# Kernel optimization log

Hardware: AMD Instinct MI355X
Metric: run time of the kernel (lower is better)

Reference implementation:

```python
import jax, jax.numpy as jnp
import numpy as np

N, NB, NP, T = 1024, 16, 256, 80
EPS_LEN = 1e-9   # seg_len clamp_min in original
EPS_DD = 1e-12   # dot(d,d) clamp_min in original


def setup_inputs() -> dict:
    key = jax.random.key(0)
    k1, k2, k3, k4 = jax.random.split(key, 4)
    # smooth-ish random trajectory (cumsum of steps)
    selected_traj = jnp.cumsum(jax.random.normal(k1, (N, T, 3), jnp.float32) * 0.5, axis=1)
    # random polylines per (sample, boundary)
    road_points = jnp.cumsum(jax.random.normal(k2, (N, NB, NP, 3), jnp.float32) * 0.5, axis=2) \
                  + jax.random.normal(k3, (N, NB, 1, 3), jnp.float32) * 2.0
    # ragged valid-prefix masks, length in [2, NP]
    lengths = jax.random.randint(k4, (N, NB), 2, NP + 1)
    road_mask = jnp.arange(NP)[None, None, :] < lengths[:, :, None]
    return {"selected_traj": selected_traj, "road_points": road_points, "road_mask": road_mask}


def _arc_project(pos, rp, rm):
    # pos: [N,T,3]; rp: [N,NB,NP,3]; rm: [N,NB,NP] bool
    n, t = pos.shape[0], pos.shape[1]
    nb, npts = rp.shape[1], rp.shape[2]
    inf = jnp.asarray(jnp.inf, pos.dtype)
    ar = jnp.arange(npts)
    n_valid = rm.sum(-1)                                    # [N,NB]

    # pack valid points to the front, preserving order (== boolean-mask gather in torch)
    order = jnp.argsort(jnp.logical_not(rm), axis=-1, stable=True)
    pts_f = jnp.take_along_axis(rp, order[..., None], axis=2)      # [N,NB,NP,3]
    pack_mask = ar[None, None, :] < n_valid[:, :, None]
    pts_f = jnp.where(pack_mask[..., None], pts_f, 0.0)
    # flipped direction: reverse the valid prefix
    flip_idx = jnp.clip(n_valid[:, :, None] - 1 - ar[None, None, :], 0, npts - 1)
    pts_b = jnp.take_along_axis(pts_f, flip_idx[..., None], axis=2)
    pts_b = jnp.where(pack_mask[..., None], pts_b, 0.0)
    pts = jnp.stack([pts_f, pts_b], axis=2)                 # [N,NB,2,NP,3]

    # segment i is real iff i < n_valid-1
    seg_mask = ar[: npts - 1][None, None, None, :] < (n_valid - 1)[:, :, None, None]  # [N,NB,1,NP-1]
    seg_vec = pts[..., 1:, :] - pts[..., :-1, :]            # [N,NB,2,NP-1,3]
    seg_norm = jnp.sqrt((seg_vec ** 2).sum(-1))
    seg_len = jnp.where(seg_mask, jnp.maximum(seg_norm, EPS_LEN), 0.0)
    cum_s = jnp.concatenate([jnp.zeros_like(seg_len[..., :1]), jnp.cumsum(seg_len, -1)], -1)  # [N,NB,2,NP]
    last_idx = jnp.clip(n_valid - 1, 0, npts - 1)[:, :, None, None]
    total_s = jnp.take_along_axis(cum_s, jnp.broadcast_to(last_idx, (n, nb, 2, 1)), -1)  # [N,NB,2,1]

    # entry: project first trajectory point onto nearest valid segment
    p0 = pos[:, 0][:, None, None, None, :]                  # [N,1,1,1,3]
    a0 = pts[..., :-1, :]
    dd0 = jnp.maximum((seg_vec ** 2).sum(-1), EPS_DD)
    t0 = jnp.clip(((p0 - a0) * seg_vec).sum(-1) / dd0, 0.0, 1.0)
    q0 = a0 + t0[..., None] * seg_vec
    d2 = jnp.where(seg_mask, ((p0 - q0) ** 2).sum(-1), inf)
    seg0 = jnp.argmin(d2, -1)[..., None]                    # [N,NB,2,1]
    entry_s = jnp.take_along_axis(cum_s, seg0, -1) + jnp.take_along_axis(t0 * seg_len, seg0, -1)

    # trajectory arc-length, resample polyline at entry_s + traj arc length
    traj_seg = jnp.sqrt(((pos[:, 1:] - pos[:, :-1]) ** 2).sum(-1))
    traj_cs = jnp.concatenate([jnp.zeros_like(traj_seg[:, :1]), jnp.cumsum(traj_seg, -1)], -1)  # [N,T]
    target_s = jnp.clip(entry_s + traj_cs[:, None, None, :], 0.0, total_s)  # [N,NB,2,T]

    j = jax.vmap(lambda c, tg: jnp.searchsorted(c, tg, side='right'))(
        cum_s.reshape(-1, npts), target_s.reshape(-1, t)) - 1
    j = jnp.clip(j.reshape(n, nb, 2, t), 0, jnp.maximum(n_valid[:, :, None, None] - 2, 0))

    seg_l = jnp.take_along_axis(seg_len, j, -1)
    cs_j = jnp.take_along_axis(cum_s, j, -1)
    t_loc = jnp.clip((target_s - cs_j) / jnp.maximum(seg_l, EPS_LEN), 0.0, 1.0)
    pa = jnp.take_along_axis(pts, j[..., None], axis=3)
    pb = jnp.take_along_axis(pts, (j + 1)[..., None], axis=3)
    proj = pa + t_loc[..., None] * (pb - pa)                # [N,NB,2,T,3]

    # pick (boundary, direction) candidate with min total L2 cost
    cost = jnp.sqrt(((pos[:, None, None] - proj) ** 2).sum(-1)).sum(-1)  # [N,NB,2]
    cand_ok = (n_valid >= 2)[:, :, None]
    cost = jnp.where(cand_ok, cost, inf)
    best = jnp.argmin(cost.reshape(n, -1), -1)
    best_proj = jnp.take_along_axis(proj.reshape(n, -1, t, 3), best[:, None, None, None], axis=1)[:, 0]
    has = cand_ok.any((1, 2))
    return jnp.where(has[:, None, None], best_proj, pos)


def reference(selected_traj, road_points, road_mask):
    pos = selected_traj[..., 0:3]
    out_pos = _arc_project(pos, road_points, road_mask)
    return jnp.concatenate([out_pos, selected_traj[..., 3:]], axis=-1)
```

## Files before the change

kernel.cpp:

```cpp
#include <hip/hip_runtime.h>
#include <math.h>

#define NN 1024
#define NBB 16
#define NP 256
#define TT 80
#define EPS_LEN 1e-9f
#define EPS_DD 1e-12f

__device__ __forceinline__ float frcp(float x){ return __builtin_amdgcn_rcpf(x); }
__device__ __forceinline__ float fsq(float x){ return __builtin_amdgcn_sqrtf(x); }
__device__ __forceinline__ float rlane_f(float x, int l){
  return __builtin_bit_cast(float, __builtin_amdgcn_readlane(__builtin_bit_cast(int, x), l));
}

template<int CTRL,int RM>
__device__ __forceinline__ float dpp_add(float v){
  int t = __builtin_amdgcn_update_dpp(0, __builtin_bit_cast(int, v), CTRL, RM, 0xf, true);
  return v + __builtin_bit_cast(float, t);
}
__device__ __forceinline__ float wave_incl_scan(float v){
  v = dpp_add<0x111,0xf>(v);
  v = dpp_add<0x112,0xf>(v);
  v = dpp_add<0x114,0xf>(v);
  v = dpp_add<0x118,0xf>(v);
  v = dpp_add<0x142,0xa>(v);
  v = dpp_add<0x143,0xc>(v);
  return v;
}
__device__ __forceinline__ float wave_sum(float v){ return rlane_f(wave_incl_scan(v), 63); }
template<int CTRL,int RM>
__device__ __forceinline__ float dpp_min(float v){
  int t = __builtin_amdgcn_update_dpp(0x7f800000, __builtin_bit_cast(int,v), CTRL, RM, 0xf, false);
  return fminf(v, __builtin_bit_cast(float,t));
}
__device__ __forceinline__ float wave_min_all(float v){
  v=dpp_min<0x111,0xf>(v); v=dpp_min<0x112,0xf>(v);
  v=dpp_min<0x114,0xf>(v); v=dpp_min<0x118,0xf>(v);
  v=dpp_min<0x142,0xa>(v); v=dpp_min<0x143,0xc>(v);
  return rlane_f(v, 63);
}

__device__ __forceinline__ void lds_fence() {
  __builtin_amdgcn_wave_barrier();
  asm volatile("s_waitcnt lgkmcnt(0)" ::: "memory");
  __builtin_amdgcn_wave_barrier();
}

__device__ __forceinline__ int wave_nv(const void* mask, size_t base, int lane) {
  bool as_byte = ((const unsigned char*)mask)[1] != 0;
  int nv = 0;
  if (as_byte) {
    uchar4 v = ((const uchar4*)((const unsigned char*)mask + base))[lane];
    nv += __popcll(__ballot(v.x != 0));
    nv += __popcll(__ballot(v.y != 0));
    nv += __popcll(__ballot(v.z != 0));
    nv += __popcll(__ballot(v.w != 0));
  } else {
    int4 v = ((const int4*)((const int*)mask + base))[lane];
    nv += __popcll(__ballot(v.x != 0));
    nv += __popcll(__ballot(v.y != 0));
    nv += __popcll(__ballot(v.z != 0));
    nv += __popcll(__ballot(v.w != 0));
  }
  return nv;
}

template<bool STRICT>
__device__ __forceinline__ int count256(const float* __restrict__ cs,
                                        const float* co, float v){
  int K = 0;
  #pragma unroll
  for (int k=0;k<16;k++) K += STRICT ? (co[k] < v) : (co[k] <= v);
  int base = (K < 16 ? K : 15) * 16;
  const float4* f4 = (const float4*)(cs + base);
  float4 c0=f4[0], c1=f4[1], c2=f4[2], c3=f4[3];
  int r;
  if (STRICT)
    r = (c0.x<v)+(c0.y<v)+(c0.z<v)+(c0.w<v)+(c1.x<v)+(c1.y<v)+(c1.z<v)+(c1.w<v)
      + (c2.x<v)+(c2.y<v)+(c2.z<v)+(c2.w<v)+(c3.x<v)+(c3.y<v)+(c3.z<v)+(c3.w<v);
  else
    r = (c0.x<=v)+(c0.y<=v)+(c0.z<=v)+(c0.w<=v)+(c1.x<=v)+(c1.y<=v)+(c1.z<=v)+(c1.w<=v)
      + (c2.x<=v)+(c2.y<=v)+(c2.z<=v)+(c2.w<=v)+(c3.x<=v)+(c3.y<=v)+(c3.z<=v)+(c3.w<=v);
  return (K >= 16) ? 256 : (base + r);
}

struct SegOut {
  float cpre[4];
  float run;
  float bdf, btf; int bjf;
  float bdl, btl; int bjl;
};

template<bool NEEDMIN>
__device__ __forceinline__ void seg_pass(const float4* __restrict__ p4, int lane, int nv,
                                         float p0x, float p0y, float p0z,
                                         float* __restrict__ pts, SegOut& R) {
  const int j0 = lane * 4;
  float4 A = make_float4(0.f,0.f,0.f,0.f), B = A, C = A;
  if (j0 < nv) { A = p4[lane*3+0]; B = p4[lane*3+1]; C = p4[lane*3+2]; }
  float x[5], y[5], z[5];
  x[0]=A.x; y[0]=A.y; z[0]=A.z;
  x[1]=A.w; y[1]=B.x; z[1]=B.y;
  x[2]=B.z; y[2]=B.w; z[2]=C.x;
  x[3]=C.y; y[3]=C.z; z[3]=C.w;
  x[4]=__shfl_down(x[0],1,64); y[4]=__shfl_down(y[0],1,64); z[4]=__shfl_down(z[0],1,64);
  ((float4*)pts)[lane*3+0] = make_float4(x[0],y[0],z[0],x[1]);
  ((float4*)pts)[lane*3+1] = make_float4(y[1],z[1],x[2],y[2]);
  ((float4*)pts)[lane*3+2] = make_float4(z[2],x[3],y[3],z[3]);
  float run = 0.f;
  R.bdf=INFINITY; R.btf=0.f; R.bjf=j0;
  R.bdl=INFINITY; R.btl=0.f; R.bjl=j0;
  #pragma unroll
  for (int k=0;k<4;k++){
    bool valid = (j0+k) < nv-1;
    float vx=x[k+1]-x[k], vy=y[k+1]-y[k], vz=z[k+1]-z[k];
    float n2 = vx*vx+vy*vy+vz*vz;
    float sl = valid ? fmaxf(fsq(n2), EPS_LEN) : 0.f;
    if (NEEDMIN){
      float t = ((p0x-x[k])*vx+(p0y-y[k])*vy+(p0z-z[k])*vz) * frcp(fmaxf(n2,EPS_DD));
      t = fminf(fmaxf(t,0.f),1.f);
      float qx=x[k]+t*vx, qy=y[k]+t*vy, qz=z[k]+t*vz;
      float dx=p0x-qx, dy=p0y-qy, dz=p0z-qz;
      float d2 = valid ? (dx*dx+dy*dy+dz*dz) : INFINITY;
      if (d2 <  R.bdf){R.bdf=d2; R.bjf=j0+k; R.btf=t;}
      if (d2 <= R.bdl){R.bdl=d2; R.bjl=j0+k; R.btl=t;}
    }
    run += sl; R.cpre[k]=run;
  }
  R.run = run;
}

__device__ __forceinline__ void cs_pair_from_regs(int idx, float ex, const SegOut& R,
                                                  float& c0, float& c1){
  int o = idx >> 2, r = idx & 3;
  float a0 = (r==0)?0.f : (r==1)?R.cpre[0] : (r==2)?R.cpre[1] : R.cpre[2];
  float a1 = (r==0)?R.cpre[0] : (r==1)?R.cpre[1] : (r==2)?R.cpre[2] : R.run;
  c0 = rlane_f(ex + a0, o);
  c1 = rlane_f(ex + a1, o);
}

__device__ __forceinline__ void interp_at(const float* __restrict__ pts,
                                          const float* __restrict__ cs,
                                          const float* co, float Tot, int nv, int jmaxv,
                                          int dir, float ts,
                                          float& prx, float& pry, float& prz){
  int ia, ib; float tl;
  if (dir){
    float v = Tot - ts;
    int lb = count256<true>(cs, co, v);
    int j = nv-1-lb; j = j<0?0:(j>jmaxv?jmaxv:j);
    int l2 = nv-1-j;
    float base = Tot - cs[l2];
    tl = (ts-base)*frcp(fmaxf(cs[l2]-cs[l2-1], EPS_LEN));
    ia=l2; ib=l2-1;
  } else {
    int ub = count256<false>(cs, co, ts);
    int j = ub-1; j = j<0?0:(j>jmaxv?jmaxv:j);
    tl = (ts - cs[j])*frcp(fmaxf(cs[j+1]-cs[j], EPS_LEN));
    ia=j; ib=j+1;
  }
  tl = fminf(fmaxf(tl,0.f),1.f);
  float3 PA = *(const float3*)(pts + ia*3);
  float3 PB = *(const float3*)(pts + ib*3);
  prx = PA.x + tl*(PB.x-PA.x);
  pry = PA.y + tl*(PB.y-PA.y);
  prz = PA.z + tl*(PB.z-PA.z);
}

__device__ void eval_cost_wave(float* __restrict__ pts, float* __restrict__ cs,
                               const float* __restrict__ pos, const float* __restrict__ tc,
                               const float4* __restrict__ p4, int nv,
                               float* __restrict__ cost2, float2* __restrict__ ent2){
  const int lane = threadIdx.x & 63;
  float l_tc[3];
  #pragma unroll
  for (int p=0;p<3;p++){
    int task = p*64 + lane;
    int r = task>=TT ? task-TT : task;
    int t = (r<TT) ? r : 0;
    l_tc[p] = tc[t];
  }
  SegOut R;
  seg_pass<true>(p4, lane, nv, pos[0], pos[1], pos[2], pts, R);

  float inc = wave_incl_scan(R.run);
  float ex = inc - R.run;
  ((float4*)cs)[lane] = make_float4(ex, ex+R.cpre[0], ex+R.cpre[1], ex+R.cpre[2]);
  const float Tot = rlane_f(inc, 63);

  float cval = ex + R.cpre[2];
  float co[16];
  #pragma unroll
  for (int k=0;k<16;k++) co[k] = rlane_f(cval, 4*k+3);

  float minv = wave_min_all(R.bdf);
  unsigned long long mf = __ballot(R.bdf == minv);
  unsigned long long ml = __ballot(R.bdl == minv);
  int lf = __builtin_ctzll(mf);
  int ll = 63 - __builtin_clzll(ml);
  int   jf = __builtin_amdgcn_readlane(R.bjf, lf);
  float tf = rlane_f(R.btf, lf);
  int   jl = __builtin_amdgcn_readlane(R.bjl, ll);
  float tl0 = rlane_f(R.btl, ll);

  float cjf, cjf1, cjl, cjl1;
  cs_pair_from_regs(jf, ex, R, cjf, cjf1);
  cs_pair_from_regs(jl, ex, R, cjl, cjl1);
  float e0 = cjf + tf*(cjf1-cjf);
  float e1 = (Tot - cjl1) + (1.f-tl0)*(cjl1-cjl);

  lds_fence();

  const int jmaxv = nv-2;
  float accf=0.f, accr=0.f;
  #pragma unroll
  for (int p=0;p<3;p++){
    int task = p*64 + lane;
    bool act = task < 2*TT;
    int dir = task>=TT ? 1 : 0;
    int t = dir ? task-TT : task;
    float ts = (dir ? e1 : e0) + l_tc[p];
    ts = fminf(fmaxf(ts,0.f),Tot);
    float prx,pry,prz;
    interp_at(pts, cs, co, Tot, nv, jmaxv, dir, ts, prx,pry,prz);
    if (act){
      float dx=pos[t*3+0]-prx, dy=pos[t*3+1]-pry, dz=pos[t*3+2]-prz;
      float dd=fsq(dx*dx+dy*dy+dz*dz);
      if (dir) accr+=dd; else accf+=dd;
    }
  }
  float cf = wave_sum(accf), cr = wave_sum(accr);
  if (lane==0){
    cost2[0]=cf; cost2[1]=cr;
    *ent2 = make_float2(e0, e1);
  }
}

__device__ void eval_proj_wave(float* __restrict__ pts, float* __restrict__ cs,
                               const float* __restrict__ tc,
                               const float4* __restrict__ p4, int nv,
                               int wdir, float entry, float* __restrict__ out){
  const int lane = threadIdx.x & 63;
  float l_tc[2];
  #pragma unroll
  for (int p=0;p<2;p++){
    int t = p*64 + lane;
    l_tc[p] = tc[(t<TT)?t:0];
  }
  SegOut R;
  seg_pass<false>(p4, lane, nv, 0.f,0.f,0.f, pts, R);
  float inc = wave_incl_scan(R.run);
  float ex = inc - R.run;
  ((float4*)cs)[lane] = make_float4(ex, ex+R.cpre[0], ex+R.cpre[1], ex+R.cpre[2]);
  const float Tot = rlane_f(inc, 63);
  float cval = ex + R.cpre[2];
  float co[16];
  #pragma unroll
  for (int k=0;k<16;k++) co[k] = rlane_f(cval, 4*k+3);
  lds_fence();
  const int jmaxv = nv-2;
  #pragma unroll
  for (int p=0;p<2;p++){
    int t = p*64 + lane;
    float ts = entry + l_tc[p];
    ts = fminf(fmaxf(ts,0.f),Tot);
    float prx,pry,prz;
    interp_at(pts, cs, co, Tot, nv, jmaxv, wdir, ts, prx,pry,prz);
    if (t < TT){ out[t*3+0]=prx; out[t*3+1]=pry; out[t*3+2]=prz; }
  }
}

__global__ __launch_bounds__(256)
void traj_cs_kernel(const float* __restrict__ traj, float* __restrict__ tcs) {
  const int wid = threadIdx.x>>6, lane = threadIdx.x&63;
  const int n = blockIdx.x*4 + wid;
  const float* p = traj + (size_t)n*TT*3;
  float* o = tcs + (size_t)n*TT;
  float dx=p[(lane+1)*3+0]-p[lane*3+0];
  float dy=p[(lane+1)*3+1]-p[lane*3+1];
  float dz=p[(lane+1)*3+2]-p[lane*3+2];
  float sA = sqrtf(dx*dx+dy*dy+dz*dz);
  float incA = sA;
  #pragma unroll
  for (int d=1;d<64;d<<=1){ float ov=__shfl_up(incA,d,64); if(lane>=d) incA+=ov; }
  o[lane+1] = incA;
  float tot = __shfl(incA, 63, 64);
  float sB = 0.f;
  if (lane<15){
    int t = 64+lane;
    float ex=p[(t+1)*3+0]-p[t*3+0];
    float ey=p[(t+1)*3+1]-p[t*3+1];
    float ez=p[(t+1)*3+2]-p[t*3+2];
    sB = sqrtf(ex*ex+ey*ey+ez*ez);
  }
  float incB = sB;
  #pragma unroll
  for (int d=1;d<64;d<<=1){ float ov=__shfl_up(incB,d,64); if(lane>=d) incB+=ov; }
  if (lane<15) o[65+lane] = tot + incB;
  if (lane==0) o[0] = 0.f;
}

__global__ __launch_bounds__(256, 8)
void fused_cost_kernel(const float* __restrict__ traj, const float* __restrict__ rp,
                       const void* __restrict__ mask, const float* __restrict__ tcs,
                       float* __restrict__ cost, float2* __restrict__ ent) {
  __shared__ float s_pts[4][NP*3], s_cs[4][NP];
  const int wid = threadIdx.x>>6, lane = threadIdx.x&63;
  const int nb = blockIdx.x*4 + wid;
  const int n = nb / NBB;
  int nvr = wave_nv(mask, (size_t)nb*NP, lane);
  if (nvr < 2){
    if (lane==0){ cost[nb*2+0]=INFINITY; cost[nb*2+1]=INFINITY; }
    return;
  }
  eval_cost_wave(s_pts[wid], s_cs[wid],
                 traj+(size_t)n*TT*3, tcs+(size_t)n*TT,
                 (const float4*)(rp+(size_t)nb*NP*3), nvr,
                 cost+(size_t)nb*2, ent+nb);
}

__global__ __launch_bounds__(256)
void winner_kernel(const float* __restrict__ traj, const float* __restrict__ rp,
                   const void* __restrict__ mask, const float* __restrict__ tcs,
                   const float* __restrict__ cost, const float2* __restrict__ ent,
                   float* __restrict__ out) {
  __shared__ float s_pts[4][NP*3], s_cs[4][NP];
  const int wid = threadIdx.x>>6, lane = threadIdx.x&63;
  const int n = blockIdx.x*4 + wid;
  const float* c = cost + (size_t)n*NBB*2;
  float bc = (lane<NBB*2) ? c[lane] : INFINITY;
  int bi = (lane<NBB*2) ? lane : 64;
  #pragma unroll
  for (int d=1;d<64;d<<=1){
    float oc=__shfl_xor(bc,d,64); int oi=__shfl_xor(bi,d,64);
    if (oc<bc || (oc==bc && oi<bi)){bc=oc;bi=oi;}
  }
  const float* pos = traj + (size_t)n*TT*3;
  float* o = out + (size_t)n*TT*3;
  if (bc == INFINITY){
    if (lane < 60) ((float4*)o)[lane] = ((const float4*)pos)[lane];
    return;
  }
  int b = bi>>1, dir = bi&1;
  const size_t nbi = (size_t)n*NBB + b;
  float2 eW = ent[nbi];
  float entry = dir ? eW.y : eW.x;
  int nv = wave_nv(mask, nbi*NP, lane);
  nv = max(nv, 2);
  eval_proj_wave(s_pts[wid], s_cs[wid], tcs+(size_t)n*TT,
                 (const float4*)(rp+nbi*NP*3), nv, dir, entry, o);
}

extern "C" void kernel_launch(void* const* d_in, const int* in_sizes, int n_in,
                              void* d_out, int out_size, void* d_ws, size_t ws_size,
                              hipStream_t stream) {
  const float* traj = (const float*)d_in[0];
  const float* rp   = (const float*)d_in[1];
  const void*  mask = d_in[2];
  float* tcs  = (float*)d_ws;
  float* cost = tcs + (size_t)NN * TT;
  float2* ent = (float2*)(cost + (size_t)NN*NBB*2);
  float* out  = (float*)d_out;

  hipLaunchKernelGGL(traj_cs_kernel, dim3(NN/4), dim3(256), 0, stream, traj, tcs);
  hipLaunchKernelGGL(fused_cost_kernel, dim3(NN*NBB/4), dim3(256), 0, stream,
                     traj, rp, mask, tcs, cost, ent);
  hipLaunchKernelGGL(winner_kernel, dim3(NN/4), dim3(256), 0, stream,
                     traj, rp, mask, tcs, cost, ent, out);
}
```

Before: 34.91 us.

## Fuse trajectory arc-length scan into cost and winner kernels, hoist road loads

Drops the separate traj_cs_kernel. Each wave now recomputes the trajectory cumulative arc length into shared memory, using a DPP scan, inside both the cost and winner kernels, which removes one launch and a global workspace round trip. Road-point float4 loads are issued unconditionally, before the mask count, so their latency overlaps it. interp_at is unified into a single strict-count path that uses a float bit bump instead of a <= comparison, which removes direction branches. The cost is redundant trajectory scanning: 16 times per sample in the cost kernel and once more in the winner kernel.

```diff
diff --git a/kernel.cpp b/kernel.cpp
--- a/kernel.cpp
+++ b/kernel.cpp
@@ -12,6 +12,9 @@
 __device__ __forceinline__ float fsq(float x){ return __builtin_amdgcn_sqrtf(x); }
 __device__ __forceinline__ float rlane_f(float x, int l){
   return __builtin_bit_cast(float, __builtin_amdgcn_readlane(__builtin_bit_cast(int, x), l));
+}
+__device__ __forceinline__ float bump(float v){
+  return __builtin_bit_cast(float, __builtin_bit_cast(int, v) + 1);
 }
 
 template<int CTRL,int RM>
@@ -66,22 +69,16 @@
   return nv;
 }
 
-template<bool STRICT>
-__device__ __forceinline__ int count256(const float* __restrict__ cs,
-                                        const float* co, float v){
+__device__ __forceinline__ int count256s(const float* __restrict__ cs,
+                                         const float* co, float v){
   int K = 0;
   #pragma unroll
-  for (int k=0;k<16;k++) K += STRICT ? (co[k] < v) : (co[k] <= v);
+  for (int k=0;k<16;k++) K += (co[k] < v);
   int base = (K < 16 ? K : 15) * 16;
   const float4* f4 = (const float4*)(cs + base);
   float4 c0=f4[0], c1=f4[1], c2=f4[2], c3=f4[3];
-  int r;
-  if (STRICT)
-    r = (c0.x<v)+(c0.y<v)+(c0.z<v)+(c0.w<v)+(c1.x<v)+(c1.y<v)+(c1.z<v)+(c1.w<v)
-      + (c2.x<v)+(c2.y<v)+(c2.z<v)+(c2.w<v)+(c3.x<v)+(c3.y<v)+(c3.z<v)+(c3.w<v);
-  else
-    r = (c0.x<=v)+(c0.y<=v)+(c0.z<=v)+(c0.w<=v)+(c1.x<=v)+(c1.y<=v)+(c1.z<=v)+(c1.w<=v)
-      + (c2.x<=v)+(c2.y<=v)+(c2.z<=v)+(c2.w<=v)+(c3.x<=v)+(c3.y<=v)+(c3.z<=v)+(c3.w<=v);
+  int r = (c0.x<v)+(c0.y<v)+(c0.z<v)+(c0.w<v)+(c1.x<v)+(c1.y<v)+(c1.z<v)+(c1.w<v)
+        + (c2.x<v)+(c2.y<v)+(c2.z<v)+(c2.w<v)+(c3.x<v)+(c3.y<v)+(c3.z<v)+(c3.w<v);
   return (K >= 16) ? 256 : (base + r);
 }
 
@@ -93,12 +90,11 @@
 };
 
 template<bool NEEDMIN>
-__device__ __forceinline__ void seg_pass(const float4* __restrict__ p4, int lane, int nv,
+__device__ __forceinline__ void seg_pass(float4 A, float4 B, float4 C,
+                                         int lane, int nv,
                                          float p0x, float p0y, float p0z,
                                          float* __restrict__ pts, SegOut& R) {
   const int j0 = lane * 4;
-  float4 A = make_float4(0.f,0.f,0.f,0.f), B = A, C = A;
-  if (j0 < nv) { A = p4[lane*3+0]; B = p4[lane*3+1]; C = p4[lane*3+2]; }
   float x[5], y[5], z[5];
   x[0]=A.x; y[0]=A.y; z[0]=A.z;
   x[1]=A.w; y[1]=B.x; z[1]=B.y;
@@ -136,7 +132,7 @@
   int o = idx >> 2, r = idx & 3;
   float a0 = (r==0)?0.f : (r==1)?R.cpre[0] : (r==2)?R.cpre[1] : R.cpre[2];
   float a1 = (r==0)?R.cpre[0] : (r==1)?R.cpre[1] : (r==2)?R.cpre[2] : R.run;
-  c0 = rlane_f(ex + a0, o);
+  c0 = rlane_f(ex + a0, idx >> 2);
   c1 = rlane_f(ex + a1, o);
 }
 
@@ -145,21 +141,16 @@
                                           const float* co, float Tot, int nv, int jmaxv,
                                           int dir, float ts,
                                           float& prx, float& pry, float& prz){
-  int ia, ib; float tl;
-  if (dir){
-    float v = Tot - ts;
-    int lb = count256<true>(cs, co, v);
-    int j = nv-1-lb; j = j<0?0:(j>jmaxv?jmaxv:j);
-    int l2 = nv-1-j;
-    float base = Tot - cs[l2];
-    tl = (ts-base)*frcp(fmaxf(cs[l2]-cs[l2-1], EPS_LEN));
-    ia=l2; ib=l2-1;
-  } else {
-    int ub = count256<false>(cs, co, ts);
-    int j = ub-1; j = j<0?0:(j>jmaxv?jmaxv:j);
-    tl = (ts - cs[j])*frcp(fmaxf(cs[j+1]-cs[j], EPS_LEN));
-    ia=j; ib=j+1;
-  }
+  float vq = dir ? (Tot - ts) : bump(ts);
+  int cnt = count256s(cs, co, vq);
+  int j = dir ? (nv-1-cnt) : (cnt-1);
+  j = j<0?0:(j>jmaxv?jmaxv:j);
+  int ia = dir ? (nv-1-j) : j;
+  int ib = dir ? (nv-2-j) : (j+1);
+  int lo = dir ? ib : ia;
+  float c_lo = cs[lo], c_hi = cs[lo+1];
+  float base = dir ? (Tot - c_hi) : c_lo;
+  float tl = (ts - base) * frcp(fmaxf(c_hi - c_lo, EPS_LEN));
   tl = fminf(fmaxf(tl,0.f),1.f);
   float3 PA = *(const float3*)(pts + ia*3);
   float3 PB = *(const float3*)(pts + ib*3);
@@ -168,25 +159,60 @@
   prz = PA.z + tl*(PB.z-PA.z);
 }
 
-__device__ void eval_cost_wave(float* __restrict__ pts, float* __restrict__ cs,
-                               const float* __restrict__ pos, const float* __restrict__ tc,
-                               const float4* __restrict__ p4, int nv,
-                               float* __restrict__ cost2, float2* __restrict__ ent2){
-  const int lane = threadIdx.x & 63;
-  float l_tc[3];
-  #pragma unroll
-  for (int p=0;p<3;p++){
-    int task = p*64 + lane;
-    int r = task>=TT ? task-TT : task;
-    int t = (r<TT) ? r : 0;
-    l_tc[p] = tc[t];
-  }
+__device__ __forceinline__ void traj_tcs_wave(const float* __restrict__ pos, int lane,
+                                              float* __restrict__ s_tc,
+                                              float3& ptl, float3& pB){
+  ptl.x = pos[lane*3+0]; ptl.y = pos[lane*3+1]; ptl.z = pos[lane*3+2];
+  pB = make_float3(0.f,0.f,0.f);
+  if (lane < 16){
+    int t = 64+lane;
+    pB.x = pos[t*3+0]; pB.y = pos[t*3+1]; pB.z = pos[t*3+2];
+  }
+  float nx = __shfl_down(ptl.x,1,64), ny = __shfl_down(ptl.y,1,64), nz = __shfl_down(ptl.z,1,64);
+  float bx0 = rlane_f(pB.x,0), by0 = rlane_f(pB.y,0), bz0 = rlane_f(pB.z,0);
+  if (lane==63){ nx=bx0; ny=by0; nz=bz0; }
+  float dx=nx-ptl.x, dy=ny-ptl.y, dz=nz-ptl.z;
+  float segA = fsq(dx*dx+dy*dy+dz*dz);
+  float mx = __shfl_down(pB.x,1,64), my = __shfl_down(pB.y,1,64), mz = __shfl_down(pB.z,1,64);
+  float ex=mx-pB.x, ey=my-pB.y, ez=mz-pB.z;
+  float segB = (lane<15) ? fsq(ex*ex+ey*ey+ez*ez) : 0.f;
+  float incA = wave_incl_scan(segA);
+  float totA = rlane_f(incA, 63);
+  float incB = wave_incl_scan(segB);
+  s_tc[lane+1] = incA;
+  if (lane<15) s_tc[65+lane] = totA + incB;
+  if (lane==0) s_tc[0] = 0.f;
+}
+
+__global__ __launch_bounds__(256, 8)
+void cost_kernel(const float* __restrict__ traj, const float* __restrict__ rp,
+                 const void* __restrict__ mask,
+                 float* __restrict__ cost, float2* __restrict__ ent) {
+  __shared__ float s_pts[4][NP*3], s_cs[4][NP], s_tc[4][TT];
+  const int wid = threadIdx.x>>6, lane = threadIdx.x&63;
+  const int nb = blockIdx.x*4 + wid;
+  const int n = nb >> 4;
+  const float* pos = traj + (size_t)n*TT*3;
+
+  const float4* p4 = (const float4*)(rp + (size_t)nb*NP*3);
+  float4 A = p4[lane*3+0], B = p4[lane*3+1], C = p4[lane*3+2];
+  int nvr = wave_nv(mask, (size_t)nb*NP, lane);
+  float3 ptl, pB;
+  traj_tcs_wave(pos, lane, s_tc[wid], ptl, pB);
+
+  if (nvr < 2){
+    if (lane==0){ cost[nb*2+0]=INFINITY; cost[nb*2+1]=INFINITY; }
+    return;
+  }
+  const int nv = nvr;
+  float p0x = rlane_f(ptl.x,0), p0y = rlane_f(ptl.y,0), p0z = rlane_f(ptl.z,0);
+
   SegOut R;
-  seg_pass<true>(p4, lane, nv, pos[0], pos[1], pos[2], pts, R);
+  seg_pass<true>(A,B,C, lane, nv, p0x,p0y,p0z, s_pts[wid], R);
 
   float inc = wave_incl_scan(R.run);
   float ex = inc - R.run;
-  ((float4*)cs)[lane] = make_float4(ex, ex+R.cpre[0], ex+R.cpre[1], ex+R.cpre[2]);
+  ((float4*)s_cs[wid])[lane] = make_float4(ex, ex+R.cpre[0], ex+R.cpre[1], ex+R.cpre[2]);
   const float Tot = rlane_f(inc, 63);
 
   float cval = ex + R.cpre[2];
@@ -203,7 +229,6 @@
   float tf = rlane_f(R.btf, lf);
   int   jl = __builtin_amdgcn_readlane(R.bjl, ll);
   float tl0 = rlane_f(R.btl, ll);
-
   float cjf, cjf1, cjl, cjl1;
   cs_pair_from_regs(jf, ex, R, cjf, cjf1);
   cs_pair_from_regs(jl, ex, R, cjl, cjl1);
@@ -212,6 +237,9 @@
 
   lds_fence();
 
+  const float* cs = s_cs[wid];
+  const float* pts = s_pts[wid];
+  const float* tcw = s_tc[wid];
   const int jmaxv = nv-2;
   float accf=0.f, accr=0.f;
   #pragma unroll
@@ -220,112 +248,36 @@
     bool act = task < 2*TT;
     int dir = task>=TT ? 1 : 0;
     int t = dir ? task-TT : task;
-    float ts = (dir ? e1 : e0) + l_tc[p];
+    int tr = t < TT ? t : TT-1;
+    float ts = (dir ? e1 : e0) + tcw[tr];
     ts = fminf(fmaxf(ts,0.f),Tot);
     float prx,pry,prz;
     interp_at(pts, cs, co, Tot, nv, jmaxv, dir, ts, prx,pry,prz);
-    if (act){
-      float dx=pos[t*3+0]-prx, dy=pos[t*3+1]-pry, dz=pos[t*3+2]-prz;
+    if (p==0){
+      float dx=ptl.x-prx, dy=ptl.y-pry, dz=ptl.z-prz;
+      accf += fsq(dx*dx+dy*dy+dz*dz);
+    } else if (act){
+      float px_, py_, pz_;
+      if (p==1 && !dir){ px_=pB.x; py_=pB.y; pz_=pB.z; }
+      else { px_=pos[t*3+0]; py_=pos[t*3+1]; pz_=pos[t*3+2]; }
+      float dx=px_-prx, dy=py_-pry, dz=pz_-prz;
       float dd=fsq(dx*dx+dy*dy+dz*dz);
       if (dir) accr+=dd; else accf+=dd;
     }
   }
   float cf = wave_sum(accf), cr = wave_sum(accr);
   if (lane==0){
-    cost2[0]=cf; cost2[1]=cr;
-    *ent2 = make_float2(e0, e1);
-  }
-}
-
-__device__ void eval_proj_wave(float* __restrict__ pts, float* __restrict__ cs,
-                               const float* __restrict__ tc,
-                               const float4* __restrict__ p4, int nv,
-                               int wdir, float entry, float* __restrict__ out){
-  const int lane = threadIdx.x & 63;
-  float l_tc[2];
-  #pragma unroll
-  for (int p=0;p<2;p++){
-    int t = p*64 + lane;
-    l_tc[p] = tc[(t<TT)?t:0];
-  }
-  SegOut R;
-  seg_pass<false>(p4, lane, nv, 0.f,0.f,0.f, pts, R);
-  float inc = wave_incl_scan(R.run);
-  float ex = inc - R.run;
-  ((float4*)cs)[lane] = make_float4(ex, ex+R.cpre[0], ex+R.cpre[1], ex+R.cpre[2]);
-  const float Tot = rlane_f(inc, 63);
-  float cval = ex + R.cpre[2];
-  float co[16];
-  #pragma unroll
-  for (int k=0;k<16;k++) co[k] = rlane_f(cval, 4*k+3);
-  lds_fence();
-  const int jmaxv = nv-2;
-  #pragma unroll
-  for (int p=0;p<2;p++){
-    int t = p*64 + lane;
-    float ts = entry + l_tc[p];
-    ts = fminf(fmaxf(ts,0.f),Tot);
-    float prx,pry,prz;
-    interp_at(pts, cs, co, Tot, nv, jmaxv, wdir, ts, prx,pry,prz);
-    if (t < TT){ out[t*3+0]=prx; out[t*3+1]=pry; out[t*3+2]=prz; }
-  }
-}
-
-__global__ __launch_bounds__(256)
-void traj_cs_kernel(const float* __restrict__ traj, float* __restrict__ tcs) {
-  const int wid = threadIdx.x>>6, lane = threadIdx.x&63;
-  const int n = blockIdx.x*4 + wid;
-  const float* p = traj + (size_t)n*TT*3;
-  float* o = tcs + (size_t)n*TT;
-  float dx=p[(lane+1)*3+0]-p[lane*3+0];
-  float dy=p[(lane+1)*3+1]-p[lane*3+1];
-  float dz=p[(lane+1)*3+2]-p[lane*3+2];
-  float sA = sqrtf(dx*dx+dy*dy+dz*dz);
-  float incA = sA;
-  #pragma unroll
-  for (int d=1;d<64;d<<=1){ float ov=__shfl_up(incA,d,64); if(lane>=d) incA+=ov; }
-  o[lane+1] = incA;
-  float tot = __shfl(incA, 63, 64);
-  float sB = 0.f;
-  if (lane<15){
-    int t = 64+lane;
-    float ex=p[(t+1)*3+0]-p[t*3+0];
-    float ey=p[(t+1)*3+1]-p[t*3+1];
-    float ez=p[(t+1)*3+2]-p[t*3+2];
-    sB = sqrtf(ex*ex+ey*ey+ez*ez);
-  }
-  float incB = sB;
-  #pragma unroll
-  for (int d=1;d<64;d<<=1){ float ov=__shfl_up(incB,d,64); if(lane>=d) incB+=ov; }
-  if (lane<15) o[65+lane] = tot + incB;
-  if (lane==0) o[0] = 0.f;
-}
-
-__global__ __launch_bounds__(256, 8)
-void fused_cost_kernel(const float* __restrict__ traj, const float* __restrict__ rp,
-                       const void* __restrict__ mask, const float* __restrict__ tcs,
-                       float* __restrict__ cost, float2* __restrict__ ent) {
-  __shared__ float s_pts[4][NP*3], s_cs[4][NP];
-  const int wid = threadIdx.x>>6, lane = threadIdx.x&63;
-  const int nb = blockIdx.x*4 + wid;
-  const int n = nb / NBB;
-  int nvr = wave_nv(mask, (size_t)nb*NP, lane);
-  if (nvr < 2){
-    if (lane==0){ cost[nb*2+0]=INFINITY; cost[nb*2+1]=INFINITY; }
-    return;
-  }
-  eval_cost_wave(s_pts[wid], s_cs[wid],
-                 traj+(size_t)n*TT*3, tcs+(size_t)n*TT,
-                 (const float4*)(rp+(size_t)nb*NP*3), nvr,
-                 cost+(size_t)nb*2, ent+nb);
+    cost[nb*2+0]=cf; cost[nb*2+1]=cr;
+    ent[nb] = make_float2(e0, e1);
+  }
 }
 
 __global__ __launch_bounds__(256)
 void winner_kernel(const float* __restrict__ traj, const float* __restrict__ rp,
-                   const void* __restrict__ mask, const float* __restrict__ tcs,
+                   const void* __restrict__ mask,
                    const float* __restrict__ cost, const float2* __restrict__ ent,
                    float* __restrict__ out) {
-  __shared__ float s_pts[4][NP*3], s_cs[4][NP];
+  __shared__ float s_pts[4][NP*3], s_cs[4][NP], s_tc[4][TT];
   const int wid = threadIdx.x>>6, lane = threadIdx.x&63;
   const int n = blockIdx.x*4 + wid;
   const float* c = cost + (size_t)n*NBB*2;
@@ -344,12 +296,42 @@
   }
   int b = bi>>1, dir = bi&1;
   const size_t nbi = (size_t)n*NBB + b;
+  const float4* p4 = (const float4*)(rp + nbi*NP*3);
+  float4 A = p4[lane*3+0], B = p4[lane*3+1], C = p4[lane*3+2];
   float2 eW = ent[nbi];
   float entry = dir ? eW.y : eW.x;
   int nv = wave_nv(mask, nbi*NP, lane);
   nv = max(nv, 2);
-  eval_proj_wave(s_pts[wid], s_cs[wid], tcs+(size_t)n*TT,
-                 (const float4*)(rp+nbi*NP*3), nv, dir, entry, o);
+  float3 ptl, pB;
+  traj_tcs_wave(pos, lane, s_tc[wid], ptl, pB);
+
+  SegOut R;
+  seg_pass<false>(A,B,C, lane, nv, 0.f,0.f,0.f, s_pts[wid], R);
+  float inc = wave_incl_scan(R.run);
+  float ex = inc - R.run;
+  ((float4*)s_cs[wid])[lane] = make_float4(ex, ex+R.cpre[0], ex+R.cpre[1], ex+R.cpre[2]);
+  const float Tot = rlane_f(inc, 63);
+  float cval = ex + R.cpre[2];
+  float co[16];
+  #pragma unroll
+  for (int k=0;k<16;k++) co[k] = rlane_f(cval, 4*k+3);
+
+  lds_fence();
+
+  const float* cs = s_cs[wid];
+  const float* pts = s_pts[wid];
+  const float* tcw = s_tc[wid];
+  const int jmaxv = nv-2;
+  #pragma unroll
+  for (int p=0;p<2;p++){
+    int t = p*64 + lane;
+    int tr = t < TT ? t : TT-1;
+    float ts = entry + tcw[tr];
+    ts = fminf(fmaxf(ts,0.f),Tot);
+    float prx,pry,prz;
+    interp_at(pts, cs, co, Tot, nv, jmaxv, dir, ts, prx,pry,prz);
+    if (t < TT){ o[t*3+0]=prx; o[t*3+1]=pry; o[t*3+2]=prz; }
+  }
 }
 
 extern "C" void kernel_launch(void* const* d_in, const int* in_sizes, int n_in,
@@ -358,14 +340,12 @@
   const float* traj = (const float*)d_in[0];
   const float* rp   = (const float*)d_in[1];
   const void*  mask = d_in[2];
-  float* tcs  = (float*)d_ws;
-  float* cost = tcs + (size_t)NN * TT;
+  float* cost = (float*)d_ws;
   float2* ent = (float2*)(cost + (size_t)NN*NBB*2);
   float* out  = (float*)d_out;
 
-  hipLaunchKernelGGL(traj_cs_kernel, dim3(NN/4), dim3(256), 0, stream, traj, tcs);
-  hipLaunchKernelGGL(fused_cost_kernel, dim3(NN*NBB/4), dim3(256), 0, stream,
-                     traj, rp, mask, tcs, cost, ent);
+  hipLaunchKernelGGL(cost_kernel, dim3(NN*NBB/4), dim3(256), 0, stream,
+                     traj, rp, mask, cost, ent);
   hipLaunchKernelGGL(winner_kernel, dim3(NN/4), dim3(256), 0, stream,
-                     traj, rp, mask, tcs, cost, ent, out);
-}
+                     traj, rp, mask, cost, ent, out);
+}
```

New measurement: 31.94 us. 8.5% less time.
